# Performance work log

Hardware: AMD Instinct MI355X
Metric: run time of the kernel (lower is better)

Reference implementation:

```python
import jax, jax.numpy as jnp
import numpy as np

B, C, H, W = 4, 96, 48, 48
N_STATE = 16
EXPAND = 2
D_INNER = EXPAND * C          # 192
DT_RANK = -(-C // 16)         # ceil(96/16) = 6
K = 4                         # 4 scan directions (VMamba cross-scan)
CA_R = 16                     # channel-attention reduction


def _ln(x, g, b, eps=1e-5):
    m = jnp.mean(x, -1, keepdims=True)
    v = jnp.mean((x - m) ** 2, -1, keepdims=True)
    return (x - m) * jax.lax.rsqrt(v + eps) * g + b


def setup_inputs() -> dict:
    key = jax.random.key(0)
    ks = jax.random.split(key, 12)
    f = lambda k, s, scale=0.02: jax.random.normal(k, s, dtype=jnp.float32) * scale
    # dt bias init per SS2D.dt_init: inv_dt = dt + log(-expm1(-dt))
    dt0 = jnp.exp(jax.random.uniform(ks[7], (K, D_INNER)) * (np.log(0.1) - np.log(1e-3)) + np.log(1e-3))
    dt_b = dt0 + jnp.log(-jnp.expm1(-dt0))
    A_logs = jnp.log(jnp.tile(jnp.arange(1, N_STATE + 1, dtype=jnp.float32)[None, :], (K * D_INNER, 1)))
    return {
        "x": jax.random.normal(ks[0], (B, C, H, W), dtype=jnp.float32),
        "ca_w1": f(ks[1], (C // CA_R, C), 0.1),
        "ca_w2": f(ks[2], (C, C // CA_R), 0.1),
        "ln_g": jnp.ones((C,), jnp.float32),
        "ln_b": jnp.zeros((C,), jnp.float32),
        "in_proj_w": f(ks[3], (2 * D_INNER, C)),
        "conv_w": f(ks[4], (D_INNER, 1, 3, 3), 0.1),
        "conv_b": jnp.zeros((D_INNER,), jnp.float32),
        "x_proj_w": f(ks[5], (K, DT_RANK + 2 * N_STATE, D_INNER)),
        "dt_w": f(ks[6], (K, D_INNER, DT_RANK), DT_RANK ** -0.5),
        "dt_b": dt_b,
        "A_logs": A_logs,
        "Ds": jnp.ones((K * D_INNER,), jnp.float32),
        "onorm_g": jnp.ones((D_INNER,), jnp.float32),
        "onorm_b": jnp.zeros((D_INNER,), jnp.float32),
        "out_proj_w": f(ks[8], (C, D_INNER)),
    }


def reference(x, ca_w1, ca_w2, ln_g, ln_b, in_proj_w, conv_w, conv_b,
              x_proj_w, dt_w, dt_b, A_logs, Ds, onorm_g, onorm_b, out_proj_w):
    # --- channel attention (SE-style) gating the encoder features ---
    s = x.mean((2, 3))                                    # [B,C]
    a = jax.nn.sigmoid(jax.nn.relu(s @ ca_w1.T) @ ca_w2.T)
    x_ca = x * a[:, :, None, None]

    # --- VSSBlock: LN -> SS2D -> residual ---
    xi = jnp.transpose(x_ca, (0, 2, 3, 1))               # [B,H,W,C]
    xn = _ln(xi, ln_g, ln_b)

    # SS2D in_proj, split x/z
    xz = xn @ in_proj_w.T                                 # [B,H,W,2*D]
    xc, z = jnp.split(xz, 2, axis=-1)

    # depthwise conv + SiLU
    xc = jnp.transpose(xc, (0, 3, 1, 2))                  # [B,D,H,W]
    xc = jax.lax.conv_general_dilated(
        xc, conv_w, (1, 1), 'SAME', feature_group_count=D_INNER,
        dimension_numbers=('NCHW', 'OIHW', 'NCHW')) + conv_b[None, :, None, None]
    xc = jax.nn.silu(xc)

    Bb, D, Hh, Ww = xc.shape
    L = Hh * Ww
    # cross-scan: hw, wh, and their reverses -> [B,4,D,L]
    x_hw = xc.reshape(Bb, D, L)
    x_wh = jnp.transpose(xc, (0, 1, 3, 2)).reshape(Bb, D, L)
    xs = jnp.stack([x_hw, x_wh], axis=1)
    xs = jnp.concatenate([xs, jnp.flip(xs, axis=-1)], axis=1)

    x_dbl = jnp.einsum('bkdl,kcd->bkcl', xs, x_proj_w)    # [B,4,R+2N,L]
    dts, Bs, Cs = jnp.split(x_dbl, [DT_RANK, DT_RANK + N_STATE], axis=2)
    dt = jnp.einsum('bkrl,kdr->bkdl', dts, dt_w)
    dt = jax.nn.softplus(dt + dt_b[None, :, :, None])     # [B,4,D,L]
    A = -jnp.exp(A_logs).reshape(K, D, N_STATE)           # [4,D,N]

    # selective scan over L (sequential recurrence, vectorized over B,K,D,N)
    dt_t = jnp.moveaxis(dt, -1, 0)                        # [L,B,4,D]
    B_t = jnp.moveaxis(Bs, -1, 0)                         # [L,B,4,N]
    C_t = jnp.moveaxis(Cs, -1, 0)
    u_t = jnp.moveaxis(xs, -1, 0)                         # [L,B,4,D]
    h0 = jnp.zeros((Bb, K, D, N_STATE), xc.dtype)

    def step(h, inp):
        dti, Bi, Ci, ui = inp
        h = h * jnp.exp(dti[..., None] * A) + (dti * ui)[..., None] * Bi[:, :, None, :]
        return h, jnp.einsum('bkdn,bkn->bkd', h, Ci)

    _, ys = jax.lax.scan(step, h0, (dt_t, B_t, C_t, u_t))
    ys = jnp.moveaxis(ys, 0, -1) + Ds.reshape(K, D)[None, :, :, None] * xs  # [B,4,D,L]

    # merge 4 directions back to hw order
    y_fwd, y_inv = ys[:, :2], jnp.flip(ys[:, 2:], axis=-1)

    def wh_to_hw(t):
        return jnp.transpose(t.reshape(Bb, D, Ww, Hh), (0, 1, 3, 2)).reshape(Bb, D, L)

    y = y_fwd[:, 0] + y_inv[:, 0] + wh_to_hw(y_fwd[:, 1]) + wh_to_hw(y_inv[:, 1])
    y = jnp.transpose(y.reshape(Bb, D, Hh, Ww), (0, 2, 3, 1))  # [B,H,W,D]
    y = _ln(y, onorm_g, onorm_b)
    y = y * jax.nn.silu(z)
    out = y @ out_proj_w.T                                # [B,H,W,C]
    out = xi + out                                        # VSSBlock residual
    return jnp.transpose(out, (0, 3, 1, 2))               # [B,C,H,W]
```

## Files before the change

kernel.cpp:

```cpp
#include <hip/hip_runtime.h>
#include <math.h>

#define Bn 4
#define Cc 96
#define Hh 48
#define Ww 48
#define HW 2304
#define Dd 192
#define NS 16
#define Kk 4
#define RK 6
#define CD 38
#define Ll 2304
#define NCH 32
#define CL 72
#define SU2S 72

typedef _Float16 half2v __attribute__((ext_vector_type(2)));
typedef _Float16 half4 __attribute__((ext_vector_type(4)));
typedef _Float16 half8 __attribute__((ext_vector_type(8)));
typedef float f4v __attribute__((ext_vector_type(4)));
typedef float f4raw __attribute__((ext_vector_type(4)));

#define FMA4(A,W,U) { A.x=fmaf(W,U.x,A.x); A.y=fmaf(W,U.y,A.y); A.z=fmaf(W,U.z,A.z); A.w=fmaf(W,U.w,A.w); }

__device__ __forceinline__ float sigmoidf_(float x){ return 1.0f/(1.0f+__expf(-x)); }
__device__ __forceinline__ float siluf_(float x){ return x*sigmoidf_(x); }
__device__ __forceinline__ float softplus_fast(float x){ return (x>15.0f)? x : __logf(1.0f+__expf(x)); }

__device__ __forceinline__ float dot2f(half2v a, half2v b, float c){
#if __has_builtin(__builtin_amdgcn_fdot2)
  return __builtin_amdgcn_fdot2(a, b, c, false);
#else
  return fmaf((float)a[1],(float)b[1], fmaf((float)a[0],(float)b[0], c));
#endif
}

__global__ __launch_bounds__(256) void k_mean(const float* __restrict__ x, float* __restrict__ s){
  int bc = blockIdx.x;
  const float* p = x + (size_t)bc*HW;
  float acc = 0.f;
  for(int i=threadIdx.x;i<HW;i+=256) acc += p[i];
  __shared__ float red[256];
  red[threadIdx.x]=acc; __syncthreads();
  for(int o=128;o>0;o>>=1){ if(threadIdx.x<o) red[threadIdx.x]+=red[threadIdx.x+o]; __syncthreads(); }
  if(threadIdx.x==0) s[bc]=red[0]*(1.0f/HW);
}

__global__ __launch_bounds__(384) void k_ca(const float* __restrict__ s, const float* __restrict__ w1,
                     const float* __restrict__ w2, float* __restrict__ a){
  __shared__ float hid[Bn*RK];
  int tid=threadIdx.x;
  if(tid<Bn*RK){
    int b=tid/RK, r=tid%RK;
    float acc=0.f;
    for(int c=0;c<Cc;c++) acc += s[b*Cc+c]*w1[r*Cc+c];
    hid[tid]=fmaxf(acc,0.f);
  }
  __syncthreads();
  int b=tid/Cc, c=tid%Cc;
  float acc=0.f;
  for(int r=0;r<RK;r++) acc += hid[b*RK+r]*w2[c*RK+r];
  a[tid]=sigmoidf_(acc);
}

__global__ __launch_bounds__(256) void k_xca(const float* __restrict__ x, const float* __restrict__ a,
                      float* __restrict__ xi){
  __shared__ float tile[32][65];
  int p0 = blockIdx.x*64, c0 = blockIdx.y*32, b = blockIdx.z;
  int pj = threadIdx.x%64, ci = threadIdx.x/64;
  for(int i=0;i<8;i++){
    int c = c0+ci+i*4;
    tile[ci+i*4][pj] = x[((size_t)(b*Cc+c))*HW + p0+pj]*a[b*Cc+c];
  }
  __syncthreads();
  int cl = threadIdx.x%32, pl = threadIdx.x/32;
  for(int i=0;i<8;i++){
    int p = pl + i*8;
    xi[((size_t)(b*HW + p0+p))*Cc + c0+cl] = tile[cl][p];
  }
}

__global__ __launch_bounds__(256) void k_lnproj(const float* __restrict__ xi,
    const float* __restrict__ g, const float* __restrict__ bta,
    const float* __restrict__ w, float* __restrict__ xc, float* __restrict__ z){
  __shared__ float su[Cc*36];
  __shared__ _Float16 wl16[128*104];
  int tid = threadIdx.x;
  int pix0 = blockIdx.x*32;
  int p = blockIdx.y;
  #pragma unroll
  for(int i=0;i<3;i++){
    int f4 = tid + 256*i;
    int px = f4/24, c4 = f4%24;
    float4 v = *(const float4*)(xi + (size_t)(pix0+px)*Cc + 4*c4);
    int sw = 4*(c4&7);
    su[(4*c4+0)*36 + (px^sw)] = v.x;
    su[(4*c4+1)*36 + (px^sw)] = v.y;
    su[(4*c4+2)*36 + (px^sw)] = v.z;
    su[(4*c4+3)*36 + (px^sw)] = v.w;
  }
  __syncthreads();
  {
    int px = tid>>3, gg = tid&7;
    float sm=0.f, sq=0.f;
    float vals[12];
    #pragma unroll
    for(int i=0;i<12;i++){
      int d = gg + 8*i;
      float v = su[d*36 + (px ^ (4*((d>>2)&7)))];
      vals[i]=v; sm+=v; sq+=v*v;
    }
    sm += __shfl_xor(sm,1); sq += __shfl_xor(sq,1);
    sm += __shfl_xor(sm,2); sq += __shfl_xor(sq,2);
    sm += __shfl_xor(sm,4); sq += __shfl_xor(sq,4);
    float mean = sm*(1.0f/Cc);
    float var  = sq*(1.0f/Cc) - mean*mean;
    float rs = rsqrtf(var + 1e-5f);
    #pragma unroll
    for(int i=0;i<12;i++){
      int d = gg + 8*i;
      su[d*36 + (px ^ (4*((d>>2)&7)))] = (vals[i]-mean)*rs*g[d] + bta[d];
    }
  }
  #pragma unroll
  for(int i=0;i<12;i++){
    int f4 = tid + 256*i;
    int r = f4/24, c4 = f4%24;
    float4 v = *(const float4*)(w + (size_t)(128*p + r)*Cc + 4*c4);
    half4 hv; hv[0]=(_Float16)v.x; hv[1]=(_Float16)v.y; hv[2]=(_Float16)v.z; hv[3]=(_Float16)v.w;
    *(half4*)(wl16 + r*104 + 4*c4) = hv;
  }
  __syncthreads();
  int t4 = tid&7, cg = tid>>3;
  float4 a0={0,0,0,0},a1={0,0,0,0},a2={0,0,0,0},a3={0,0,0,0};
  for(int d0=0; d0<Cc; d0+=8){
    half8 w0v = *(const half8*)(wl16 + (cg+  0)*104 + d0);
    half8 w1v = *(const half8*)(wl16 + (cg+ 32)*104 + d0);
    half8 w2v = *(const half8*)(wl16 + (cg+ 64)*104 + d0);
    half8 w3v = *(const half8*)(wl16 + (cg+ 96)*104 + d0);
    #pragma unroll
    for(int j=0;j<8;j++){
      int d = d0+j;
      float4 u4 = *(const float4*)(su + d*36 + 4*(t4 ^ ((d>>2)&7)));
      FMA4(a0,(float)w0v[j],u4);
      FMA4(a1,(float)w1v[j],u4);
      FMA4(a2,(float)w2v[j],u4);
      FMA4(a3,(float)w3v[j],u4);
    }
  }
  #pragma unroll
  for(int j=0;j<4;j++){
    int c = 128*p + cg + 32*j;
    float4 a = (j==0)?a0:(j==1)?a1:(j==2)?a2:a3;
    #pragma unroll
    for(int q=0;q<4;q++){
      int px = pix0 + 4*t4 + q;
      float vv = (q==0)?a.x:(q==1)?a.y:(q==2)?a.z:a.w;
      if(c < Dd) xc[(size_t)px*Dd + c] = vv;
      else       z [(size_t)px*Dd + (c-Dd)] = vv;
    }
  }
}

__global__ __launch_bounds__(256) void k_conv(const float* __restrict__ xc, const float* __restrict__ cw,
                       const float* __restrict__ cb, float* __restrict__ xo){
  int idx = blockIdx.x*256 + threadIdx.x;
  if(idx >= Bn*HW*(Dd/4)) return;
  int d4 = idx % (Dd/4); int pos = (idx/(Dd/4))%HW; int b = idx/((Dd/4)*HW);
  int h = pos/Ww, w = pos%Ww;
  int d0 = d4*4;
  float4 acc = {cb[d0],cb[d0+1],cb[d0+2],cb[d0+3]};
  #pragma unroll
  for(int kh=0;kh<3;kh++){
    int hh=h+kh-1; if(hh<0||hh>=Hh) continue;
    #pragma unroll
    for(int kw=0;kw<3;kw++){
      int ww2=w+kw-1; if(ww2<0||ww2>=Ww) continue;
      float4 v = *(const float4*)(xc + ((size_t)(b*HW + hh*Ww+ww2))*Dd + d0);
      int wi = kh*3+kw;
      acc.x += v.x*cw[(d0+0)*9+wi];
      acc.y += v.y*cw[(d0+1)*9+wi];
      acc.z += v.z*cw[(d0+2)*9+wi];
      acc.w += v.w*cw[(d0+3)*9+wi];
    }
  }
  float4 o; o.x=siluf_(acc.x); o.y=siluf_(acc.y); o.z=siluf_(acc.z); o.w=siluf_(acc.w);
  *(float4*)(xo + ((size_t)(b*HW+pos))*Dd + d0) = o;
}

__global__ __launch_bounds__(256) void k_xdbl(const float* __restrict__ xconv,
   const float* __restrict__ xpw, const float* __restrict__ dtw,
   const float* __restrict__ dtb, _Float16* __restrict__ dtT,
   _Float16* __restrict__ uT, _Float16* __restrict__ BC){
  __shared__ _Float16 su2[96*SU2S];
  __shared__ _Float16 wl16[CD*200];
  __shared__ float dts[RK*36];
  int tid = threadIdx.x;
  int blk = blockIdx.x;
  int tile = blk % (Ll/32);
  int k    = (blk/(Ll/32))%Kk;
  int b    = blk/((Ll/32)*Kk);
  int ord  = k&1;
  bool rev = (k>=2);
  int t0 = tile*32;
  #pragma unroll
  for(int i=0;i<6;i++){
    int f4 = tid+256*i;
    int r = f4/48, c4 = f4%48;
    int t = t0+r;
    int pos = ord ? ((t%Ww)*Ww + t/Ww) : t;
    float4 v = *(const float4*)(xconv + (size_t)(b*HW+pos)*Dd + 4*c4);
    int dp0 = 2*c4;
    int off = ((r>>2) ^ (c4&7))*8 + (r&3)*2;
    half2v p0; p0[0]=(_Float16)v.x; p0[1]=(_Float16)v.y;
    half2v p1; p1[0]=(_Float16)v.z; p1[1]=(_Float16)v.w;
    *(half2v*)(su2 + dp0*SU2S + off) = p0;
    *(half2v*)(su2 + (dp0+1)*SU2S + off) = p1;
  }
  for(int i=tid;i<CD*48;i+=256){
    int c = i/48, c4 = i%48;
    float4 v = *(const float4*)(xpw + ((size_t)(k*CD+c))*Dd + 4*c4);
    half4 hv; hv[0]=(_Float16)v.x; hv[1]=(_Float16)v.y; hv[2]=(_Float16)v.z; hv[3]=(_Float16)v.w;
    *(half4*)(wl16 + c*200 + 4*c4) = hv;
  }
  __syncthreads();
  if(k<2 && tid < Dd){
    int d = tid;
    int dp = d>>1, par = d&1, swz = (dp>>1)&7;
    _Float16* up = uT + ((size_t)(b*2+ord)*Dd + d)*Ll + t0;
    #pragma unroll
    for(int r4=0;r4<8;r4++){
      half8 hv = *(const half8*)(su2 + dp*SU2S + (r4 ^ swz)*8);
      half4 o; o[0]=hv[0+par]; o[1]=hv[2+par]; o[2]=hv[4+par]; o[3]=hv[6+par];
      *(half4*)(up + 4*r4) = o;
    }
  }
  int t4 = tid&7, cg = tid>>3;
  bool has1 = (cg < CD-32);
  f4v a0={0,0,0,0}, a1={0,0,0,0};
  #pragma unroll 1
  for(int dpc=0; dpc<24; dpc++){
    f4raw w0r = *(const f4raw*)(wl16 + cg*200 + 8*dpc);
    f4raw w1r = {0.f,0.f,0.f,0.f};
    if(has1) w1r = *(const f4raw*)(wl16 + (cg+32)*200 + 8*dpc);
    #pragma unroll
    for(int j=0;j<4;j++){
      int dp = 4*dpc+j;
      f4raw ur = *(const f4raw*)(su2 + dp*SU2S + (t4 ^ ((dp>>1)&7))*8);
      half2v w0p = __builtin_bit_cast(half2v, w0r[j]);
      half2v w1p = __builtin_bit_cast(half2v, w1r[j]);
      #pragma unroll
      for(int q=0;q<4;q++){
        half2v up = __builtin_bit_cast(half2v, ur[q]);
        a0[q] = dot2f(up, w0p, a0[q]);
        if(has1) a1[q] = dot2f(up, w1p, a1[q]);
      }
    }
  }
  #pragma unroll
  for(int j=0;j<2;j++){
    if(j==1 && !has1) break;
    int c = cg + 32*j;
    f4v a = j? a1 : a0;
    if(c < RK){
      dts[c*36 + 4*t4+0]=a[0]; dts[c*36+4*t4+1]=a[1]; dts[c*36+4*t4+2]=a[2]; dts[c*36+4*t4+3]=a[3];
    } else {
      int nn = c - RK;
      _Float16* dst = BC + ((size_t)(b*Kk+k)*Ll)*32 + nn;
      #pragma unroll
      for(int q=0;q<4;q++){
        int t = t0 + 4*t4 + q;
        int tq = rev ? (Ll-1-t) : t;
        dst[(size_t)tq*32] = (_Float16)a[q];
      }
    }
  }
  __syncthreads();
  int tl = tid&31, ds8 = tid>>5;
  #pragma unroll 4
  for(int i=0;i<24;i++){
    int d = ds8 + 8*i;
    float acc = dtb[k*Dd + d];
    #pragma unroll
    for(int r=0;r<RK;r++) acc = fmaf(dtw[((size_t)(k*Dd+d))*RK + r], dts[r*36 + tl], acc);
    acc = softplus_fast(acc);
    int tq = rev ? (Ll-1-t0-tl) : (t0+tl);
    dtT[((size_t)(b*Kk+k)*Dd + d)*Ll + tq] = (_Float16)acc;
  }
}

__global__ __launch_bounds__(192) void k_scan1(const _Float16* __restrict__ dtT,
  const _Float16* __restrict__ uT, const _Float16* __restrict__ BC,
  const float* __restrict__ Alog, float* __restrict__ hloc, float* __restrict__ Pb){
  int blk=blockIdx.x;
  int ch  = blk%NCH;
  int k   = (blk/NCH)%Kk;
  int b   = blk/(NCH*Kk);
  int d = threadIdx.x;
  const float* ap = Alog + ((size_t)(k*Dd+d))*NS;
  float An[16];
  #pragma unroll
  for(int i=0;i<16;i++) An[i] = -__expf(ap[i]);
  const _Float16* dp = dtT + ((size_t)(b*Kk+k)*Dd + d)*Ll + ch*CL;
  const _Float16* ub = uT  + ((size_t)(b*2+(k&1))*Dd + d)*Ll;
  const _Float16* bc = BC  + ((size_t)(b*Kk+k)*Ll + ch*CL)*32;
  bool rev = (k>=2);
  int s0 = ch*CL;
  float h[16];
  #pragma unroll
  for(int i=0;i<16;i++) h[i]=0.f;
  float sdt = 0.f;
  #pragma unroll 1
  for(int tl=0; tl<CL; tl+=4){
    half4 dt4 = *(const half4*)(dp+tl);
    float u[4];
    if(!rev){
      half4 u4 = *(const half4*)(ub + s0+tl);
      u[0]=(float)u4[0]; u[1]=(float)u4[1]; u[2]=(float)u4[2]; u[3]=(float)u4[3];
    } else {
      half4 u4 = *(const half4*)(ub + (Ll-4-s0-tl));
      u[0]=(float)u4[3]; u[1]=(float)u4[2]; u[2]=(float)u4[1]; u[3]=(float)u4[0];
    }
    #pragma unroll
    for(int j=0;j<4;j++){
      half8 B0 = *(const half8*)(bc + (size_t)(tl+j)*32);
      half8 B1 = *(const half8*)(bc + (size_t)(tl+j)*32 + 8);
      float dtv = (float)dt4[j];
      sdt += dtv;
      float xB = dtv*u[j];
      #pragma unroll
      for(int i=0;i<8;i++){
        float ae = __expf(dtv*An[i]);
        h[i] = fmaf(h[i], ae, xB*(float)B0[i]);
      }
      #pragma unroll
      for(int i=0;i<8;i++){
        float ae = __expf(dtv*An[8+i]);
        h[8+i] = fmaf(h[8+i], ae, xB*(float)B1[i]);
      }
    }
  }
  size_t o = (((size_t)(b*Kk+k)*NCH + ch)*Dd + d)*NS;
  f4v h0={h[0],h[1],h[2],h[3]}, h1={h[4],h[5],h[6],h[7]};
  f4v h2={h[8],h[9],h[10],h[11]}, h3={h[12],h[13],h[14],h[15]};
  *(f4v*)(hloc+o)=h0; *(f4v*)(hloc+o+4)=h1; *(f4v*)(hloc+o+8)=h2; *(f4v*)(hloc+o+12)=h3;
  float P[16];
  #pragma unroll
  for(int i=0;i<16;i++) P[i] = __expf(An[i]*sdt);
  f4v p0={P[0],P[1],P[2],P[3]}, p1={P[4],P[5],P[6],P[7]};
  f4v p2={P[8],P[9],P[10],P[11]}, p3={P[12],P[13],P[14],P[15]};
  *(f4v*)(Pb+o)=p0; *(f4v*)(Pb+o+4)=p1; *(f4v*)(Pb+o+8)=p2; *(f4v*)(Pb+o+12)=p3;
}

__global__ __launch_bounds__(256) void k_comb(float* __restrict__ hloc,
  const float* __restrict__ Pb){
  int idx = blockIdx.x*256 + threadIdx.x;
  int inner = idx % (Dd*NS);
  int bk = idx / (Dd*NS);
  size_t base = (size_t)bk*NCH*Dd*NS + inner;
  float H = 0.f;
  for(int ch=0; ch<NCH; ch++){
    size_t o = base + (size_t)ch*Dd*NS;
    float hl = hloc[o];
    hloc[o] = H;
    H = Pb[o]*H + hl;
  }
}

__global__ __launch_bounds__(192) void k_scan2(const _Float16* __restrict__ dtT,
  const _Float16* __restrict__ uT, const _Float16* __restrict__ BC,
  const float* __restrict__ Alog, const float* __restrict__ Ds,
  const float* __restrict__ Hin, _Float16* __restrict__ yB){
  int blk=blockIdx.x;
  int ch  = blk%NCH;
  int k   = (blk/NCH)%Kk;
  int b   = blk/(NCH*Kk);
  int d = threadIdx.x;
  const float* ap = Alog + ((size_t)(k*Dd+d))*NS;
  float An[16];
  #pragma unroll
  for(int i=0;i<16;i++) An[i] = -__expf(ap[i]);
  float Dv = Ds[k*Dd+d];
  const _Float16* dp = dtT + ((size_t)(b*Kk+k)*Dd + d)*Ll + ch*CL;
  const _Float16* ub = uT  + ((size_t)(b*2+(k&1))*Dd + d)*Ll;
  const _Float16* bc = BC  + ((size_t)(b*Kk+k)*Ll + ch*CL)*32;
  bool rev = (k>=2);
  int s0 = ch*CL;
  const float* hp = Hin + (((size_t)(b*Kk+k)*NCH + ch)*Dd + d)*NS;
  float h[16];
  {
    f4v h0=*(const f4v*)(hp), h1=*(const f4v*)(hp+4), h2=*(const f4v*)(hp+8), h3=*(const f4v*)(hp+12);
    h[0]=h0[0];h[1]=h0[1];h[2]=h0[2];h[3]=h0[3];
    h[4]=h1[0];h[5]=h1[1];h[6]=h1[2];h[7]=h1[3];
    h[8]=h2[0];h[9]=h2[1];h[10]=h2[2];h[11]=h2[3];
    h[12]=h3[0];h[13]=h3[1];h[14]=h3[2];h[15]=h3[3];
  }
  _Float16* yp = yB + ((size_t)(b*Kk+k)*Ll + s0)*Dd + d;
  #pragma unroll 1
  for(int tl=0; tl<CL; tl+=4){
    half4 dt4 = *(const half4*)(dp+tl);
    float u[4];
    if(!rev){
      half4 u4 = *(const half4*)(ub + s0+tl);
      u[0]=(float)u4[0]; u[1]=(float)u4[1]; u[2]=(float)u4[2]; u[3]=(float)u4[3];
    } else {
      half4 u4 = *(const half4*)(ub + (Ll-4-s0-tl));
      u[0]=(float)u4[3]; u[1]=(float)u4[2]; u[2]=(float)u4[1]; u[3]=(float)u4[0];
    }
    #pragma unroll
    for(int j=0;j<4;j++){
      half8 B0 = *(const half8*)(bc + (size_t)(tl+j)*32);
      half8 B1 = *(const half8*)(bc + (size_t)(tl+j)*32 + 8);
      half8 C0 = *(const half8*)(bc + (size_t)(tl+j)*32 + 16);
      half8 C1 = *(const half8*)(bc + (size_t)(tl+j)*32 + 24);
      float dtv = (float)dt4[j];
      float xB = dtv*u[j];
      float p = 0.f;
      #pragma unroll
      for(int i=0;i<8;i++){
        float ae = __expf(dtv*An[i]);
        h[i] = fmaf(h[i], ae, xB*(float)B0[i]);
        p = fmaf(h[i], (float)C0[i], p);
      }
      #pragma unroll
      for(int i=0;i<8;i++){
        float ae = __expf(dtv*An[8+i]);
        h[8+i] = fmaf(h[8+i], ae, xB*(float)B1[i]);
        p = fmaf(h[8+i], (float)C1[i], p);
      }
      yp[(size_t)(tl+j)*Dd] = (_Float16)(p + Dv*u[j]);
    }
  }
}

__global__ __launch_bounds__(256) void k_merge(const _Float16* __restrict__ yB,
  const float* __restrict__ og, const float* __restrict__ ob,
  const float* __restrict__ zB, const float* __restrict__ opw,
  const float* __restrict__ xi, float* __restrict__ ot){
  __shared__ float yv[Dd*36];
  __shared__ _Float16 wl16[48*200];
  int tid = threadIdx.x;
  int pix0 = blockIdx.x*32;
  int p = blockIdx.y;
  int b = pix0/HW;
  int pos0 = pix0%HW;
  size_t ybase = (size_t)b*Kk*Ll*Dd;
  #pragma unroll
  for(int i=0;i<3;i++){
    int f8 = tid+256*i;
    int r = f8/24, c8 = f8%24;
    int pos = pos0+r;
    int lwh = (pos%Ww)*Ww + pos/Ww;
    half8 v0 = *(const half8*)(yB + ybase + ((size_t)(0*Ll) + pos)*Dd + 8*c8);
    half8 v2 = *(const half8*)(yB + ybase + ((size_t)(2*Ll) + (Ll-1-pos))*Dd + 8*c8);
    half8 v1 = *(const half8*)(yB + ybase + ((size_t)(1*Ll) + lwh)*Dd + 8*c8);
    half8 v3 = *(const half8*)(yB + ybase + ((size_t)(3*Ll) + (Ll-1-lwh))*Dd + 8*c8);
    #pragma unroll
    for(int j=0;j<8;j++){
      int d = 8*c8+j;
      float vs = (float)v0[j]+(float)v1[j]+(float)v2[j]+(float)v3[j];
      yv[d*36 + (r ^ (4*((d>>2)&7)))] = vs;
    }
  }
  for(int i=tid;i<48*48;i+=256){
    int c=i/48, c4=i%48;
    float4 v = *(const float4*)(opw + (size_t)(48*p+c)*Dd + 4*c4);
    half4 hv; hv[0]=(_Float16)v.x; hv[1]=(_Float16)v.y; hv[2]=(_Float16)v.z; hv[3]=(_Float16)v.w;
    *(half4*)(wl16 + c*200 + 4*c4) = hv;
  }
  __syncthreads();
  {
    int px = tid>>3, gg = tid&7;
    float sm=0.f, sq=0.f;
    float vals[24];
    #pragma unroll
    for(int i=0;i<24;i++){
      int d = gg + 8*i;
      float v = yv[d*36 + (px ^ (4*((d>>2)&7)))];
      vals[i]=v; sm+=v; sq+=v*v;
    }
    sm += __shfl_xor(sm,1); sq += __shfl_xor(sq,1);
    sm += __shfl_xor(sm,2); sq += __shfl_xor(sq,2);
    sm += __shfl_xor(sm,4); sq += __shfl_xor(sq,4);
    float mean = sm*(1.0f/Dd);
    float var  = sq*(1.0f/Dd) - mean*mean;
    float rs = rsqrtf(var + 1e-5f);
    #pragma unroll
    for(int i=0;i<24;i++){
      int d = gg + 8*i;
      float zv = zB[(size_t)(pix0+px)*Dd + d];
      yv[d*36 + (px ^ (4*((d>>2)&7)))] = ((vals[i]-mean)*rs*og[d] + ob[d]) * siluf_(zv);
    }
  }
  __syncthreads();
  int t4 = tid&7, cg = tid>>3;
  bool h1 = (cg < 16);
  float4 a0={0,0,0,0}, a1={0,0,0,0};
  for(int d0=0;d0<Dd;d0+=8){
    half8 w0v = *(const half8*)(wl16 + cg*200 + d0);
    half8 w1v;
    if(h1) w1v = *(const half8*)(wl16 + (cg+32)*200 + d0);
    #pragma unroll
    for(int j=0;j<8;j++){
      int d=d0+j;
      float4 u4 = *(const float4*)(yv + d*36 + 4*(t4 ^ ((d>>2)&7)));
      FMA4(a0,(float)w0v[j],u4);
      if(h1){ FMA4(a1,(float)w1v[j],u4); }
    }
  }
  #pragma unroll
  for(int j=0;j<2;j++){
    if(j==1 && !h1) break;
    int c = 48*p + cg + 32*j;
    float4 a = j?a1:a0;
    #pragma unroll
    for(int q=0;q<4;q++){
      int px = pix0 + 4*t4 + q;
      float vv = (q==0)?a.x:(q==1)?a.y:(q==2)?a.z:a.w;
      ot[(size_t)px*Cc + c] = vv + xi[(size_t)px*Cc + c];
    }
  }
}

__global__ __launch_bounds__(256) void k_outT(const float* __restrict__ ot, float* __restrict__ out){
  __shared__ float tile[64][33];
  int p0=blockIdx.x*64, c0=blockIdx.y*32, b=blockIdx.z;
  int cl=threadIdx.x%32, pl=threadIdx.x/32;
  for(int i=0;i<8;i++){
    int p = pl+i*8;
    tile[p][cl] = ot[((size_t)(b*HW+p0+p))*Cc + c0+cl];
  }
  __syncthreads();
  int pj=threadIdx.x%64, ci=threadIdx.x/64;
  for(int i=0;i<8;i++){
    int c=ci+i*4;
    out[((size_t)(b*Cc+c0+c))*HW + p0+pj] = tile[pj][c];
  }
}

extern "C" void kernel_launch(void* const* d_in, const int* in_sizes, int n_in,
                              void* d_out, int out_size, void* d_ws, size_t ws_size,
                              hipStream_t stream){
  const float* x   = (const float*)d_in[0];
  const float* cw1 = (const float*)d_in[1];
  const float* cw2 = (const float*)d_in[2];
  const float* lng = (const float*)d_in[3];
  const float* lnb = (const float*)d_in[4];
  const float* ipw = (const float*)d_in[5];
  const float* cvw = (const float*)d_in[6];
  const float* cvb = (const float*)d_in[7];
  const float* xpw = (const float*)d_in[8];
  const float* dtw = (const float*)d_in[9];
  const float* dtb = (const float*)d_in[10];
  const float* alg = (const float*)d_in[11];
  const float* ds  = (const float*)d_in[12];
  const float* ong = (const float*)d_in[13];
  const float* onb = (const float*)d_in[14];
  const float* opw = (const float*)d_in[15];
  float* out = (float*)d_out;
  float* ws = (float*)d_ws;

  float* s_   = ws;
  float* a_   = s_  + 384;
  float* xi_  = a_  + 384;
  float* xc_  = xi_ + 884736;
  float* z_   = xc_ + 1769472;
  float* xo_  = z_  + 1769472;
  _Float16* dtT_ = (_Float16*)(xo_ + 1769472);
  _Float16* uT_  = dtT_ + 7077888;
  _Float16* BC_  = uT_ + 3538944;
  _Float16* yB_  = BC_ + 1179648;
  float* ot_  = (float*)(yB_ + 7077888);

  float* hloc_ = xc_;
  float* Pb_   = xo_;

  k_mean  <<<Bn*Cc, 256, 0, stream>>>(x, s_);
  k_ca    <<<1, 384, 0, stream>>>(s_, cw1, cw2, a_);
  k_xca   <<<dim3(HW/64, Cc/32, Bn), 256, 0, stream>>>(x, a_, xi_);
  k_lnproj<<<dim3(Bn*HW/32, 3), 256, 0, stream>>>(xi_, lng, lnb, ipw, xc_, z_);
  k_conv  <<<(Bn*HW*(Dd/4))/256, 256, 0, stream>>>(xc_, cvw, cvb, xo_);
  k_xdbl  <<<Bn*Kk*(Ll/32), 256, 0, stream>>>(xo_, xpw, dtw, dtb, dtT_, uT_, BC_);
  k_scan1 <<<Bn*Kk*NCH, 192, 0, stream>>>(dtT_, uT_, BC_, alg, hloc_, Pb_);
  k_comb  <<<(Bn*Kk*Dd*NS)/256, 256, 0, stream>>>(hloc_, Pb_);
  k_scan2 <<<Bn*Kk*NCH, 192, 0, stream>>>(dtT_, uT_, BC_, alg, ds, hloc_, yB_);
  k_merge <<<dim3(Bn*HW/32, 2), 256, 0, stream>>>(yB_, ong, onb, z_, opw, xi_, ot_);
  k_outT  <<<dim3(HW/64, Cc/32, Bn), 256, 0, stream>>>(ot_, out);
}
```

Measured before the change: 196.6 us.

## Double chunk count for scan, store chunk states in fp16, prefetch dt/u

Splits the selective scan into 64 chunks of 36 steps instead of 32 of 72, doubling the number of scan blocks to raise occupancy and shorten the serial per-block chain. Chunk-local states and decay products are stored in fp16 to halve the inter-kernel traffic that grows with the chunk count. The dt and u loads for the next step group are issued one iteration ahead to hide memory latency. This adds a longer serial combine over 64 chunks and loses precision in the carried states and decay products.

```diff
diff --git a/kernel.cpp b/kernel.cpp
--- a/kernel.cpp
+++ b/kernel.cpp
@@ -12,8 +12,8 @@
 #define RK 6
 #define CD 38
 #define Ll 2304
-#define NCH 32
-#define CL 72
+#define NCH 64
+#define CL 36
 #define SU2S 72
 
 typedef _Float16 half2v __attribute__((ext_vector_type(2)));
@@ -292,7 +292,7 @@
 
 __global__ __launch_bounds__(192) void k_scan1(const _Float16* __restrict__ dtT,
   const _Float16* __restrict__ uT, const _Float16* __restrict__ BC,
-  const float* __restrict__ Alog, float* __restrict__ hloc, float* __restrict__ Pb){
+  const float* __restrict__ Alog, _Float16* __restrict__ hloc, _Float16* __restrict__ Pb){
   int blk=blockIdx.x;
   int ch  = blk%NCH;
   int k   = (blk/NCH)%Kk;
@@ -311,17 +311,16 @@
   #pragma unroll
   for(int i=0;i<16;i++) h[i]=0.f;
   float sdt = 0.f;
+  half4 dt4 = *(const half4*)(dp);
+  half4 u4r = rev ? *(const half4*)(ub + (Ll-4-s0)) : *(const half4*)(ub + s0);
   #pragma unroll 1
   for(int tl=0; tl<CL; tl+=4){
-    half4 dt4 = *(const half4*)(dp+tl);
+    int tln = (tl+4<CL)? tl+4 : 0;
+    half4 dt4n = *(const half4*)(dp+tln);
+    half4 u4n  = rev ? *(const half4*)(ub + (Ll-4-s0-tln)) : *(const half4*)(ub + s0+tln);
     float u[4];
-    if(!rev){
-      half4 u4 = *(const half4*)(ub + s0+tl);
-      u[0]=(float)u4[0]; u[1]=(float)u4[1]; u[2]=(float)u4[2]; u[3]=(float)u4[3];
-    } else {
-      half4 u4 = *(const half4*)(ub + (Ll-4-s0-tl));
-      u[0]=(float)u4[3]; u[1]=(float)u4[2]; u[2]=(float)u4[1]; u[3]=(float)u4[0];
-    }
+    if(!rev){ u[0]=(float)u4r[0]; u[1]=(float)u4r[1]; u[2]=(float)u4r[2]; u[3]=(float)u4r[3]; }
+    else    { u[0]=(float)u4r[3]; u[1]=(float)u4r[2]; u[2]=(float)u4r[1]; u[3]=(float)u4r[0]; }
     #pragma unroll
     for(int j=0;j<4;j++){
       half8 B0 = *(const half8*)(bc + (size_t)(tl+j)*32);
@@ -340,21 +339,21 @@
         h[8+i] = fmaf(h[8+i], ae, xB*(float)B1[i]);
       }
     }
+    dt4 = dt4n; u4r = u4n;
   }
   size_t o = (((size_t)(b*Kk+k)*NCH + ch)*Dd + d)*NS;
-  f4v h0={h[0],h[1],h[2],h[3]}, h1={h[4],h[5],h[6],h[7]};
-  f4v h2={h[8],h[9],h[10],h[11]}, h3={h[12],h[13],h[14],h[15]};
-  *(f4v*)(hloc+o)=h0; *(f4v*)(hloc+o+4)=h1; *(f4v*)(hloc+o+8)=h2; *(f4v*)(hloc+o+12)=h3;
-  float P[16];
-  #pragma unroll
-  for(int i=0;i<16;i++) P[i] = __expf(An[i]*sdt);
-  f4v p0={P[0],P[1],P[2],P[3]}, p1={P[4],P[5],P[6],P[7]};
-  f4v p2={P[8],P[9],P[10],P[11]}, p3={P[12],P[13],P[14],P[15]};
-  *(f4v*)(Pb+o)=p0; *(f4v*)(Pb+o+4)=p1; *(f4v*)(Pb+o+8)=p2; *(f4v*)(Pb+o+12)=p3;
-}
-
-__global__ __launch_bounds__(256) void k_comb(float* __restrict__ hloc,
-  const float* __restrict__ Pb){
+  half8 ho0, ho1;
+  #pragma unroll
+  for(int i=0;i<8;i++){ ho0[i]=(_Float16)h[i]; ho1[i]=(_Float16)h[8+i]; }
+  *(half8*)(hloc+o) = ho0; *(half8*)(hloc+o+8) = ho1;
+  half8 po0, po1;
+  #pragma unroll
+  for(int i=0;i<8;i++){ po0[i]=(_Float16)__expf(An[i]*sdt); po1[i]=(_Float16)__expf(An[8+i]*sdt); }
+  *(half8*)(Pb+o) = po0; *(half8*)(Pb+o+8) = po1;
+}
+
+__global__ __launch_bounds__(256) void k_comb(_Float16* __restrict__ hloc,
+  const _Float16* __restrict__ Pb){
   int idx = blockIdx.x*256 + threadIdx.x;
   int inner = idx % (Dd*NS);
   int bk = idx / (Dd*NS);
@@ -362,16 +361,16 @@
   float H = 0.f;
   for(int ch=0; ch<NCH; ch++){
     size_t o = base + (size_t)ch*Dd*NS;
-    float hl = hloc[o];
-    hloc[o] = H;
-    H = Pb[o]*H + hl;
+    float hl = (float)hloc[o];
+    hloc[o] = (_Float16)H;
+    H = (float)Pb[o]*H + hl;
   }
 }
 
 __global__ __launch_bounds__(192) void k_scan2(const _Float16* __restrict__ dtT,
   const _Float16* __restrict__ uT, const _Float16* __restrict__ BC,
   const float* __restrict__ Alog, const float* __restrict__ Ds,
-  const float* __restrict__ Hin, _Float16* __restrict__ yB){
+  const _Float16* __restrict__ Hin, _Float16* __restrict__ yB){
   int blk=blockIdx.x;
   int ch  = blk%NCH;
   int k   = (blk/NCH)%Kk;
@@ -387,27 +386,24 @@
   const _Float16* bc = BC  + ((size_t)(b*Kk+k)*Ll + ch*CL)*32;
   bool rev = (k>=2);
   int s0 = ch*CL;
-  const float* hp = Hin + (((size_t)(b*Kk+k)*NCH + ch)*Dd + d)*NS;
+  const _Float16* hp = Hin + (((size_t)(b*Kk+k)*NCH + ch)*Dd + d)*NS;
   float h[16];
   {
-    f4v h0=*(const f4v*)(hp), h1=*(const f4v*)(hp+4), h2=*(const f4v*)(hp+8), h3=*(const f4v*)(hp+12);
-    h[0]=h0[0];h[1]=h0[1];h[2]=h0[2];h[3]=h0[3];
-    h[4]=h1[0];h[5]=h1[1];h[6]=h1[2];h[7]=h1[3];
-    h[8]=h2[0];h[9]=h2[1];h[10]=h2[2];h[11]=h2[3];
-    h[12]=h3[0];h[13]=h3[1];h[14]=h3[2];h[15]=h3[3];
+    half8 h0=*(const half8*)(hp), h1=*(const half8*)(hp+8);
+    #pragma unroll
+    for(int i=0;i<8;i++){ h[i]=(float)h0[i]; h[8+i]=(float)h1[i]; }
   }
   _Float16* yp = yB + ((size_t)(b*Kk+k)*Ll + s0)*Dd + d;
+  half4 dt4 = *(const half4*)(dp);
+  half4 u4r = rev ? *(const half4*)(ub + (Ll-4-s0)) : *(const half4*)(ub + s0);
   #pragma unroll 1
   for(int tl=0; tl<CL; tl+=4){
-    half4 dt4 = *(const half4*)(dp+tl);
+    int tln = (tl+4<CL)? tl+4 : 0;
+    half4 dt4n = *(const half4*)(dp+tln);
+    half4 u4n  = rev ? *(const half4*)(ub + (Ll-4-s0-tln)) : *(const half4*)(ub + s0+tln);
     float u[4];
-    if(!rev){
-      half4 u4 = *(const half4*)(ub + s0+tl);
-      u[0]=(float)u4[0]; u[1]=(float)u4[1]; u[2]=(float)u4[2]; u[3]=(float)u4[3];
-    } else {
-      half4 u4 = *(const half4*)(ub + (Ll-4-s0-tl));
-      u[0]=(float)u4[3]; u[1]=(float)u4[2]; u[2]=(float)u4[1]; u[3]=(float)u4[0];
-    }
+    if(!rev){ u[0]=(float)u4r[0]; u[1]=(float)u4r[1]; u[2]=(float)u4r[2]; u[3]=(float)u4r[3]; }
+    else    { u[0]=(float)u4r[3]; u[1]=(float)u4r[2]; u[2]=(float)u4r[1]; u[3]=(float)u4r[0]; }
     #pragma unroll
     for(int j=0;j<4;j++){
       half8 B0 = *(const half8*)(bc + (size_t)(tl+j)*32);
@@ -431,6 +427,7 @@
       }
       yp[(size_t)(tl+j)*Dd] = (_Float16)(p + Dv*u[j]);
     }
+    dt4 = dt4n; u4r = u4n;
   }
 }
 
@@ -573,8 +570,8 @@
   _Float16* yB_  = BC_ + 1179648;
   float* ot_  = (float*)(yB_ + 7077888);
 
-  float* hloc_ = xc_;
-  float* Pb_   = xo_;
+  _Float16* hloc_ = (_Float16*)xc_;
+  _Float16* Pb_   = (_Float16*)xo_;
 
   k_mean  <<<Bn*Cc, 256, 0, stream>>>(x, s_);
   k_ca    <<<1, 384, 0, stream>>>(s_, cw1, cw2, a_);
```

Result: slower. 244.2 us (+24.2%).
